# Kernel optimization log

Measured on AMD Instinct MI355X. Metric: run time of the kernel, lower is better.

The kernel has to match this reference:

```python
import jax, jax.numpy as jnp
import numpy as np

TAU = 250.0   # tau_inv used by all behaviours (norse default / explicit for LLBN)
DT = 0.001
VTH = 30.0
T_STEPS = 10000

# (a, b, c, d) Izhikevich params per cell
LLBN_P = (0.1, -0.075, -55.0, 6.0)      # custom spiking behaviour
EBN_P = (0.02, 0.25, -55.0, 0.05)       # phasic_bursting
IFN_P = (0.02, 0.25, -65.0, 6.0)        # phasic_spiking
TN_P = (0.02, 0.2, -65.0, 6.0)          # tonic_spiking
MN_P = (0.02, 0.25, -65.0, 6.0)         # phasic_spiking


def setup_inputs() -> dict:
    key = jax.random.key(0)
    k1, k2 = jax.random.split(key)
    input_mat = jax.random.uniform(k1, (127, 127), dtype=jnp.float32)
    weights_matrix = jax.random.uniform(k2, (12,), dtype=jnp.float32)
    return {"input_mat": input_mat, "weights_matrix": weights_matrix,
            "nb_repetitions": T_STEPS}


def _izh(v, u, I, p):
    a, b, c, d = p
    v1 = v + TAU * DT * (0.04 * v * v + 5.0 * v + 140.0 - u + I)
    u1 = u + TAU * DT * a * (b * v - u)
    z = (v1 >= VTH).astype(v.dtype)
    return z, jnp.where(z > 0, c, v1), u1 + z * d


def _simulate(input_mat, w, nb_repetitions):
    z_plus = jnp.sum(input_mat * w[0])  # constant across timesteps

    def step(carry, _):
        temp, z2p, v2, u2, v3, u3, v4, u4, z5p, v5, u5, v6, u6 = carry
        # LLBN: recurrent cell, input current = w2*(z_plus*w1 - temp) + w3*z_prev
        z2, v2, u2 = _izh(v2, u2, w[2] * (z_plus * w[1] - temp) + w[3] * z2p, LLBN_P)
        # EBN
        z3, v3, u3 = _izh(v3, u3, z_plus * w[4] + z2 * w[5], EBN_P)
        # IFN (feedback to LLBN via temp, one-step delay)
        z4, v4, u4 = _izh(v4, u4, z3 * w[6], IFN_P)
        temp_n = z4 * w[7]
        # TN: recurrent cell, input current = w9*(z3*w8) + w10*z_prev
        z5, v5, u5 = _izh(v5, u5, w[9] * (z3 * w[8]) + w[10] * z5p, TN_P)
        # MN
        z6, v6, u6 = _izh(v6, u6, z5 * w[11], MN_P)
        new_carry = (temp_n, z2, v2, u2, v3, u3, v4, u4, z5, v5, u5, v6, u6)
        out = (jnp.stack([z2, z3, z4, z5, z6]),  # spikes [5]
               jnp.stack([v2, v3, v4, v5, v6]))  # membrane voltages [5]
        return new_carry, out

    f32 = jnp.float32
    init = (f32(0.0),                      # temp
            f32(0.0), f32(-60.0), f32(4.5),    # LLBN z, v, u (u0 = b*v_rest)
            f32(-64.0), f32(-16.0),            # EBN v, u
            f32(-64.0), f32(-16.0),            # IFN v, u
            f32(0.0), f32(-70.0), f32(-14.0),  # TN z, v, u
            f32(-64.0), f32(-16.0))            # MN v, u
    _, (spikes, volts) = jax.lax.scan(step, init, None, length=nb_repetitions)
    return spikes.T, volts.T  # each [5, T]


def reference(input_mat, weights_matrix, nb_repetitions):
    o_spikes, v = _simulate(input_mat, weights_matrix, nb_repetitions)
    return o_spikes, v
```

## Files before the change

kernel.cpp:

```cpp
#include <hip/hip_runtime.h>

#pragma clang fp contract(off)


__global__ __launch_bounds__(256) void net_sim(const float* __restrict__ mat,
                                               const float* __restrict__ w,
                                               float* __restrict__ out,
                                               int* __restrict__ ws,
                                               int T) {
    __shared__ double red[256];
    const int tid = threadIdx.x;

    const float w0 = w[0];
    double s = 0.0;
    for (int i = tid; i < 127 * 127; i += 256) {
        float p = mat[i] * w0;
        s += (double)p;
    }
    red[tid] = s;
    __syncthreads();
    #pragma unroll
    for (int off = 128; off > 0; off >>= 1) {
        if (tid < off) red[tid] += red[tid + off];
        __syncthreads();
    }
    if (tid >= 9) return;

    const float z_plus = (float)red[0];

    const float w2 = w[2], w3 = w[3], w5 = w[5], w6 = w[6], w7 = w[7],
                w8 = w[8], w9 = w[9], w10 = w[10], w11 = w[11];
    const float zp_w1 = z_plus * w[1];
    const float zp_w4 = z_plus * w[4];

    const float I2_00 = w2 * (zp_w1 - 0.0f) + w3 * 0.0f;
    const float I2_10 = w2 * (zp_w1 - 0.0f) + w3 * 1.0f;
    const float I2_01 = w2 * (zp_w1 - w7)   + w3 * 0.0f;
    const float I2_11 = w2 * (zp_w1 - w7)   + w3 * 1.0f;
    const float I3_0  = zp_w4 + 0.0f * w5;
    const float I3_1  = zp_w4 + 1.0f * w5;
    const float I4_0  = 0.0f * w6;
    const float I4_1  = 1.0f * w6;
    const float I5_00 = w9 * (0.0f * w8) + w10 * 0.0f;
    const float I5_10 = w9 * (1.0f * w8) + w10 * 0.0f;
    const float I5_01 = w9 * (0.0f * w8) + w10 * 1.0f;
    const float I5_11 = w9 * (1.0f * w8) + w10 * 1.0f;
    const float I6_0  = 0.0f * w11;
    const float I6_1  = 1.0f * w11;

    const int lane = tid;
    const int g = lane == 0 ? 0 : lane <= 2 ? 1 : lane <= 4 ? 2 : lane <= 6 ? 3 : 4;

    const float ka = lane == 0 ? (float)(0.25 * 0.1) : (float)(0.25 * 0.02);
    const float b  = lane == 0 ? -0.075f : (g == 3 ? 0.2f : 0.25f);
    const float c  = g <= 1 ? -55.0f : -65.0f;
    const float d  = g == 1 ? 0.05f : 6.0f;
    float v = g == 0 ? -60.0f : (g == 3 ? -70.0f : -64.0f);
    float u = g == 0 ? 4.5f   : (g == 3 ? -14.0f : -16.0f);

    const float C0a = g == 0 ? I2_00 : g == 1 ? I3_0 : g == 2 ? I4_0
                    : g == 3 ? I5_00 : I6_0;
    const float C0b = g == 0 ? I2_00 : g == 1 ? I3_0 : g == 2 ? I4_0
                    : g == 3 ? I5_01 : I6_0;
    const float C1a = g == 1 ? I3_1 : g == 2 ? I4_1 : g == 3 ? I5_10
                    : g == 4 ? I6_1 : 0.0f;
    const float C1b = g == 1 ? I3_1 : g == 2 ? I4_1 : g == 3 ? I5_11
                    : g == 4 ? I6_1 : 0.0f;

    const bool is_lane0  = (lane == 0);
    const bool spec_var1 = (lane == 2) | (lane == 4) | (lane == 6) | (lane == 8);
    const unsigned lanebit = 1u << lane;

    float* __restrict__ psp = out + g * T;
    float* __restrict__ pvv = out + 5 * T + g * T;

    int z2 = 0, z4 = 0, z5 = 0;

    float av = 0.0f, au = 0.0f;
    int az2 = 0, az4 = 0, az5 = 0;
    int anchor_t = -1, next_anchor = 8;
    int t_det = -1, Pf = 0;

    float zb[8], vb[8];

    int t = 0;
    for (; t + 8 <= T; t += 8) {
        if (t == next_anchor) {
            av = v; au = u; az2 = z2; az4 = z4; az5 = z5;
            anchor_t = t; next_anchor <<= 1;
        } else if (anchor_t >= 0) {
            unsigned long long mv =
                __ballot(__float_as_uint(v) == __float_as_uint(av));
            unsigned long long mu =
                __ballot(__float_as_uint(u) == __float_as_uint(au));
            if (((mv & mu) & 0x1FFull) == 0x1FFull &&
                z2 == az2 && z4 == az4 && z5 == az5) {
                t_det = t; Pf = t - anchor_t;
                break;
            }
        }

        #pragma unroll
        for (int j = 0; j < 8; ++j) {
            float fI2 = z4 ? (z2 ? I2_11 : I2_01) : (z2 ? I2_10 : I2_00);
            float V0 = z5 ? C0b : C0a;
            float V1 = z5 ? C1b : C1a;
            V0 = is_lane0 ? fI2 : V0;
            float Ib = spec_var1 ? V1 : V0;

            float t1 = 0.04f * v;
            float t2 = t1 * v;
            float t3 = 5.0f * v;
            float t4 = t2 + t3;
            float t5 = t4 + 140.0f;
            float t6 = t5 - u;
            float bv = b * v;
            float bvu = bv - u;
            float du = ka * bvu;
            float u1 = u + du;

            float t7b = t6 + Ib;
            float dvb = 0.25f * t7b;
            float v1b = v + dvb;
            unsigned long long m = __ballot(v1b >= 30.0f);

            int nz2 = (int)(m & 1ull);
            int z3  = (int)((m >> (1 + nz2)) & 1ull);
            int nz4 = (int)((m >> (3 + z3)) & 1ull);
            int nz5 = (int)((m >> (5 + z3)) & 1ull);
            unsigned ssel = (nz2 ? 0x006u : 0u) | (z3 ? 0x078u : 0u)
                          | (nz5 ? 0x180u : 0u);

            bool asel = (ssel & lanebit) != 0u;
            float Ia = asel ? V1 : V0;
            float t7a = t6 + Ia;
            float dva = 0.25f * t7a;
            float v1a = v + dva;
            bool fa = (v1a >= 30.0f);
            v = fa ? c : v1a;
            float u1d = u1 + d;
            u = fa ? u1d : u1;

            zb[j] = fa ? 1.0f : 0.0f;
            vb[j] = v;

            z2 = nz2; z4 = nz4; z5 = nz5;
        }
        *(float4*)(psp)     = make_float4(zb[0], zb[1], zb[2], zb[3]);
        *(float4*)(psp + 4) = make_float4(zb[4], zb[5], zb[6], zb[7]);
        *(float4*)(pvv)     = make_float4(vb[0], vb[1], vb[2], vb[3]);
        *(float4*)(pvv + 4) = make_float4(vb[4], vb[5], vb[6], vb[7]);
        psp += 8;
        pvv += 8;
    }
    for (; t < T && t_det < 0; ++t) {
        float fI2 = z4 ? (z2 ? I2_11 : I2_01) : (z2 ? I2_10 : I2_00);
        float V0 = z5 ? C0b : C0a;
        float V1 = z5 ? C1b : C1a;
        V0 = is_lane0 ? fI2 : V0;
        float Ib = spec_var1 ? V1 : V0;
        float t1 = 0.04f * v;
        float t2 = t1 * v;
        float t3 = 5.0f * v;
        float t4 = t2 + t3;
        float t5 = t4 + 140.0f;
        float t6 = t5 - u;
        float bv = b * v;
        float bvu = bv - u;
        float du = ka * bvu;
        float u1 = u + du;
        float t7b = t6 + Ib;
        float dvb = 0.25f * t7b;
        float v1b = v + dvb;
        unsigned long long m = __ballot(v1b >= 30.0f);
        int nz2 = (int)(m & 1ull);
        int z3  = (int)((m >> (1 + nz2)) & 1ull);
        int nz4 = (int)((m >> (3 + z3)) & 1ull);
        int nz5 = (int)((m >> (5 + z3)) & 1ull);
        unsigned ssel = (nz2 ? 0x006u : 0u) | (z3 ? 0x078u : 0u)
                      | (nz5 ? 0x180u : 0u);
        bool asel = (ssel & lanebit) != 0u;
        float Ia = asel ? V1 : V0;
        float t7a = t6 + Ia;
        float dva = 0.25f * t7a;
        float v1a = v + dva;
        bool fa = (v1a >= 30.0f);
        v = fa ? c : v1a;
        float u1d = u1 + d;
        u = fa ? u1d : u1;
        psp[0] = fa ? 1.0f : 0.0f;
        pvv[0] = v;
        ++psp; ++pvv;
        z2 = nz2; z4 = nz4; z5 = nz5;
    }

    if (lane == 0) {
        ws[0] = (t_det >= 0) ? 1 : 0;
        ws[1] = t_det;
        ws[2] = Pf;
    }
}

__global__ __launch_bounds__(256) void fill_cycle(float* __restrict__ out,
                                                  const int* __restrict__ ws,
                                                  int T) {
    if (ws[0] == 0) return;
    const int t0 = ws[1];
    const int P  = ws[2];
    const int r  = blockIdx.y;
    const float* __restrict__ src = out + (size_t)r * T + (t0 - P);
    float* __restrict__ dst       = out + (size_t)r * T + t0;
    const int n = T - t0;
    for (int i = blockIdx.x * blockDim.x + threadIdx.x; i < n;
         i += gridDim.x * blockDim.x) {
        dst[i] = src[i % P];
    }
}

extern "C" void kernel_launch(void* const* d_in, const int* in_sizes, int n_in,
                              void* d_out, int out_size, void* d_ws, size_t ws_size,
                              hipStream_t stream) {
    const float* mat = (const float*)d_in[0];
    const float* w   = (const float*)d_in[1];
    int T = out_size / 10;
    net_sim<<<1, 256, 0, stream>>>(mat, w, (float*)d_out, (int*)d_ws, T);
    dim3 grid(40, 10, 1);
    fill_cycle<<<grid, 256, 0, stream>>>((float*)d_out, (const int*)d_ws, T);
}
```

Baseline: 346.1 us.

## Use one lane per cell with dual-input speculation and add periodic fine cycle anchors

Each of the 5 neurons now runs on a single lane. Every lane evaluates both possible input currents, and two ballots resolve the spike chain as scalar SGPR masks; v_cndmask inline asm then applies the selections with no per-lane recomputation. This replaces the 9-lane speculative layout and its second dependent v1 computation plus compare. Cycle detection gains a fine anchor every 64 steps alongside the doubling coarse anchor, so a periodic steady state can be found earlier and the remaining outputs filled by copying. The cost is an extra pair of ballots and compares in each 8-step check.

```diff
diff --git a/kernel.cpp b/kernel.cpp
--- a/kernel.cpp
+++ b/kernel.cpp
@@ -2,6 +2,12 @@
 
 #pragma clang fp contract(off)
 
+
+__device__ __forceinline__ float sel_mask(float a, float b, unsigned long long m) {
+    float r;
+    asm("v_cndmask_b32 %0, %1, %2, %3" : "=v"(r) : "v"(a), "v"(b), "s"(m));
+    return r;
+}
 
 __global__ __launch_bounds__(256) void net_sim(const float* __restrict__ mat,
                                                const float* __restrict__ w,
@@ -24,7 +30,7 @@
         if (tid < off) red[tid] += red[tid + off];
         __syncthreads();
     }
-    if (tid >= 9) return;
+    if (tid >= 5) return;
 
     const float z_plus = (float)red[0];
 
@@ -49,64 +55,68 @@
     const float I6_1  = 1.0f * w11;
 
     const int lane = tid;
-    const int g = lane == 0 ? 0 : lane <= 2 ? 1 : lane <= 4 ? 2 : lane <= 6 ? 3 : 4;
-
     const float ka = lane == 0 ? (float)(0.25 * 0.1) : (float)(0.25 * 0.02);
-    const float b  = lane == 0 ? -0.075f : (g == 3 ? 0.2f : 0.25f);
-    const float c  = g <= 1 ? -55.0f : -65.0f;
-    const float d  = g == 1 ? 0.05f : 6.0f;
-    float v = g == 0 ? -60.0f : (g == 3 ? -70.0f : -64.0f);
-    float u = g == 0 ? 4.5f   : (g == 3 ? -14.0f : -16.0f);
-
-    const float C0a = g == 0 ? I2_00 : g == 1 ? I3_0 : g == 2 ? I4_0
-                    : g == 3 ? I5_00 : I6_0;
-    const float C0b = g == 0 ? I2_00 : g == 1 ? I3_0 : g == 2 ? I4_0
-                    : g == 3 ? I5_01 : I6_0;
-    const float C1a = g == 1 ? I3_1 : g == 2 ? I4_1 : g == 3 ? I5_10
-                    : g == 4 ? I6_1 : 0.0f;
-    const float C1b = g == 1 ? I3_1 : g == 2 ? I4_1 : g == 3 ? I5_11
-                    : g == 4 ? I6_1 : 0.0f;
-
-    const bool is_lane0  = (lane == 0);
-    const bool spec_var1 = (lane == 2) | (lane == 4) | (lane == 6) | (lane == 8);
-    const unsigned lanebit = 1u << lane;
-
-    float* __restrict__ psp = out + g * T;
-    float* __restrict__ pvv = out + 5 * T + g * T;
+    const float b  = lane == 0 ? -0.075f : (lane == 3 ? 0.2f : 0.25f);
+    const float cc = lane <= 1 ? -55.0f : -65.0f;
+    const float d  = lane == 1 ? 0.05f : 6.0f;
+    float v = lane == 0 ? -60.0f : (lane == 3 ? -70.0f : -64.0f);
+    float u = lane == 0 ? 4.5f   : (lane == 3 ? -14.0f : -16.0f);
+
+    const float K0a = lane == 1 ? I3_0 : lane == 2 ? I4_0 : lane == 3 ? I5_00
+                    : lane == 4 ? I6_0 : 0.0f;
+    const float K0b = lane == 3 ? I5_01 : K0a;
+    const float K1a = lane == 1 ? I3_1 : lane == 2 ? I4_1 : lane == 3 ? I5_10
+                    : lane == 4 ? I6_1 : 0.0f;
+    const float K1b = lane == 3 ? I5_11 : K1a;
+    const bool is_l0 = (lane == 0);
+
+    float* __restrict__ psp = out + lane * T;
+    float* __restrict__ pvv = out + 5 * T + lane * T;
 
     int z2 = 0, z4 = 0, z5 = 0;
 
-    float av = 0.0f, au = 0.0f;
-    int az2 = 0, az4 = 0, az5 = 0;
-    int anchor_t = -1, next_anchor = 8;
+    float fav = 0.0f, fau = 0.0f; int faz2 = 0, faz4 = 0, faz5 = 0, fa_t = -1;
+    float cav = 0.0f, cau = 0.0f; int caz2 = 0, caz4 = 0, caz5 = 0, ca_t = -1;
+    int next_coarse = 8;
     int t_det = -1, Pf = 0;
 
     float zb[8], vb[8];
 
     int t = 0;
     for (; t + 8 <= T; t += 8) {
-        if (t == next_anchor) {
-            av = v; au = u; az2 = z2; az4 = z4; az5 = z5;
-            anchor_t = t; next_anchor <<= 1;
-        } else if (anchor_t >= 0) {
+        int hitA = -1;
+        if (fa_t >= 0) {
             unsigned long long mv =
-                __ballot(__float_as_uint(v) == __float_as_uint(av));
+                __ballot(__float_as_uint(v) == __float_as_uint(fav));
             unsigned long long mu =
-                __ballot(__float_as_uint(u) == __float_as_uint(au));
-            if (((mv & mu) & 0x1FFull) == 0x1FFull &&
-                z2 == az2 && z4 == az4 && z5 == az5) {
-                t_det = t; Pf = t - anchor_t;
-                break;
-            }
+                __ballot(__float_as_uint(u) == __float_as_uint(fau));
+            if (((mv & mu) & 0x1Full) == 0x1Full &&
+                z2 == faz2 && z4 == faz4 && z5 == faz5) hitA = fa_t;
+        }
+        if (hitA < 0 && ca_t >= 0) {
+            unsigned long long mv =
+                __ballot(__float_as_uint(v) == __float_as_uint(cav));
+            unsigned long long mu =
+                __ballot(__float_as_uint(u) == __float_as_uint(cau));
+            if (((mv & mu) & 0x1Full) == 0x1Full &&
+                z2 == caz2 && z4 == caz4 && z5 == caz5) hitA = ca_t;
+        }
+        if (hitA >= 0) { t_det = t; Pf = t - hitA; break; }
+        if ((t & 63) == 0 && t) {
+            fav = v; fau = u; faz2 = z2; faz4 = z4; faz5 = z5; fa_t = t;
+        }
+        if (t == next_coarse) {
+            cav = v; cau = u; caz2 = z2; caz4 = z4; caz5 = z5; ca_t = t;
+            next_coarse <<= 1;
         }
 
         #pragma unroll
         for (int j = 0; j < 8; ++j) {
             float fI2 = z4 ? (z2 ? I2_11 : I2_01) : (z2 ? I2_10 : I2_00);
-            float V0 = z5 ? C0b : C0a;
-            float V1 = z5 ? C1b : C1a;
-            V0 = is_lane0 ? fI2 : V0;
-            float Ib = spec_var1 ? V1 : V0;
+            float J0 = z5 ? K0b : K0a;
+            float J1 = z5 ? K1b : K1a;
+            J0 = is_l0 ? fI2 : J0;
+            J1 = is_l0 ? fI2 : J1;
 
             float t1 = 0.04f * v;
             float t2 = t1 * v;
@@ -118,30 +128,36 @@
             float bvu = bv - u;
             float du = ka * bvu;
             float u1 = u + du;
-
-            float t7b = t6 + Ib;
-            float dvb = 0.25f * t7b;
-            float v1b = v + dvb;
-            unsigned long long m = __ballot(v1b >= 30.0f);
-
-            int nz2 = (int)(m & 1ull);
-            int z3  = (int)((m >> (1 + nz2)) & 1ull);
-            int nz4 = (int)((m >> (3 + z3)) & 1ull);
-            int nz5 = (int)((m >> (5 + z3)) & 1ull);
-            unsigned ssel = (nz2 ? 0x006u : 0u) | (z3 ? 0x078u : 0u)
-                          | (nz5 ? 0x180u : 0u);
-
-            bool asel = (ssel & lanebit) != 0u;
-            float Ia = asel ? V1 : V0;
-            float t7a = t6 + Ia;
-            float dva = 0.25f * t7a;
-            float v1a = v + dva;
-            bool fa = (v1a >= 30.0f);
-            v = fa ? c : v1a;
             float u1d = u1 + d;
-            u = fa ? u1d : u1;
-
-            zb[j] = fa ? 1.0f : 0.0f;
+
+            float t7_0 = t6 + J0;
+            float dv_0 = 0.25f * t7_0;
+            float v1_0 = v + dv_0;
+            float t7_1 = t6 + J1;
+            float dv_1 = 0.25f * t7_1;
+            float v1_1 = v + dv_1;
+            unsigned long long m0 = __ballot(v1_0 >= 30.0f);
+            unsigned long long m1 = __ballot(v1_1 >= 30.0f);
+
+            int nz2 = (int)(m0 & 1ull);
+            unsigned long long me = nz2 ? m1 : m0;
+            int z3  = (int)((me >> 1) & 1ull);
+            unsigned long long mi = z3 ? m1 : m0;
+            int nz4 = (int)((mi >> 2) & 1ull);
+            int nz5 = (int)((mi >> 3) & 1ull);
+            unsigned long long mm = nz5 ? m1 : m0;
+            int nz6 = (int)((mm >> 4) & 1ull);
+
+            unsigned long long act = (nz2 ? 0x02ull : 0ull) |
+                                     (z3  ? 0x0Cull : 0ull) |
+                                     (nz5 ? 0x10ull : 0ull);
+            unsigned long long fam = (unsigned long long)(nz2 | (z3 << 1) |
+                                     (nz4 << 2) | (nz5 << 3) | (nz6 << 4));
+
+            float v1a = sel_mask(v1_0, v1_1, act);
+            v = sel_mask(v1a, cc, fam);
+            u = sel_mask(u1, u1d, fam);
+            zb[j] = sel_mask(0.0f, 1.0f, fam);
             vb[j] = v;
 
             z2 = nz2; z4 = nz4; z5 = nz5;
@@ -155,10 +171,10 @@
     }
     for (; t < T && t_det < 0; ++t) {
         float fI2 = z4 ? (z2 ? I2_11 : I2_01) : (z2 ? I2_10 : I2_00);
-        float V0 = z5 ? C0b : C0a;
-        float V1 = z5 ? C1b : C1a;
-        V0 = is_lane0 ? fI2 : V0;
-        float Ib = spec_var1 ? V1 : V0;
+        float J0 = z5 ? K0b : K0a;
+        float J1 = z5 ? K1b : K1a;
+        J0 = is_l0 ? fI2 : J0;
+        J1 = is_l0 ? fI2 : J1;
         float t1 = 0.04f * v;
         float t2 = t1 * v;
         float t3 = 5.0f * v;
@@ -169,26 +185,32 @@
         float bvu = bv - u;
         float du = ka * bvu;
         float u1 = u + du;
-        float t7b = t6 + Ib;
-        float dvb = 0.25f * t7b;
-        float v1b = v + dvb;
-        unsigned long long m = __ballot(v1b >= 30.0f);
-        int nz2 = (int)(m & 1ull);
-        int z3  = (int)((m >> (1 + nz2)) & 1ull);
-        int nz4 = (int)((m >> (3 + z3)) & 1ull);
-        int nz5 = (int)((m >> (5 + z3)) & 1ull);
-        unsigned ssel = (nz2 ? 0x006u : 0u) | (z3 ? 0x078u : 0u)
-                      | (nz5 ? 0x180u : 0u);
-        bool asel = (ssel & lanebit) != 0u;
-        float Ia = asel ? V1 : V0;
-        float t7a = t6 + Ia;
-        float dva = 0.25f * t7a;
-        float v1a = v + dva;
-        bool fa = (v1a >= 30.0f);
-        v = fa ? c : v1a;
         float u1d = u1 + d;
-        u = fa ? u1d : u1;
-        psp[0] = fa ? 1.0f : 0.0f;
+        float t7_0 = t6 + J0;
+        float dv_0 = 0.25f * t7_0;
+        float v1_0 = v + dv_0;
+        float t7_1 = t6 + J1;
+        float dv_1 = 0.25f * t7_1;
+        float v1_1 = v + dv_1;
+        unsigned long long m0 = __ballot(v1_0 >= 30.0f);
+        unsigned long long m1 = __ballot(v1_1 >= 30.0f);
+        int nz2 = (int)(m0 & 1ull);
+        unsigned long long me = nz2 ? m1 : m0;
+        int z3  = (int)((me >> 1) & 1ull);
+        unsigned long long mi = z3 ? m1 : m0;
+        int nz4 = (int)((mi >> 2) & 1ull);
+        int nz5 = (int)((mi >> 3) & 1ull);
+        unsigned long long mm = nz5 ? m1 : m0;
+        int nz6 = (int)((mm >> 4) & 1ull);
+        unsigned long long act = (nz2 ? 0x02ull : 0ull) |
+                                 (z3  ? 0x0Cull : 0ull) |
+                                 (nz5 ? 0x10ull : 0ull);
+        unsigned long long fam = (unsigned long long)(nz2 | (z3 << 1) |
+                                 (nz4 << 2) | (nz5 << 3) | (nz6 << 4));
+        float v1a = sel_mask(v1_0, v1_1, act);
+        v = sel_mask(v1a, cc, fam);
+        u = sel_mask(u1, u1d, fam);
+        psp[0] = sel_mask(0.0f, 1.0f, fam);
         pvv[0] = v;
         ++psp; ++pvv;
         z2 = nz2; z4 = nz4; z5 = nz5;
```

After: 328.4 us. -5.1%, faster.

## Add periodic-40 anchor for cycle detection and use SGPR-mask lane select

Applied to the files above, without the earlier changes.

Adds a second cycle-detection anchor that re-anchors every 40 steps and checks at those points, alongside the existing power-of-two anchor. This catches steady-state periods that divide 40 much earlier than the doubling anchor does, so the serial simulation can stop sooner and hand the rest to the fill kernel. It also replaces the per-lane bit test with an inline-asm v_cndmask driven by a scalar 64-bit mask, which shortens the serial critical path of each step. Risks include inline asm constraints forcing extra moves, and detection that is only valid when the state repeats exactly.

```diff
diff --git a/kernel.cpp b/kernel.cpp
--- a/kernel.cpp
+++ b/kernel.cpp
@@ -2,6 +2,12 @@
 
 #pragma clang fp contract(off)
 
+
+__device__ __forceinline__ float sel_mask(float a, float b, unsigned long long m) {
+    float r;
+    asm("v_cndmask_b32 %0, %1, %2, %3" : "=v"(r) : "v"(a), "v"(b), "s"(m));
+    return r;
+}
 
 __global__ __launch_bounds__(256) void net_sim(const float* __restrict__ mat,
                                                const float* __restrict__ w,
@@ -69,35 +75,48 @@
 
     const bool is_lane0  = (lane == 0);
     const bool spec_var1 = (lane == 2) | (lane == 4) | (lane == 6) | (lane == 8);
-    const unsigned lanebit = 1u << lane;
 
     float* __restrict__ psp = out + g * T;
     float* __restrict__ pvv = out + 5 * T + g * T;
 
     int z2 = 0, z4 = 0, z5 = 0;
 
-    float av = 0.0f, au = 0.0f;
-    int az2 = 0, az4 = 0, az5 = 0;
-    int anchor_t = -1, next_anchor = 8;
+    float rav = 0.0f, rau = 0.0f; int raz2 = 0, raz4 = 0, raz5 = 0, ra_t = -1;
+    float cav = 0.0f, cau = 0.0f; int caz2 = 0, caz4 = 0, caz5 = 0, ca_t = -1;
+    int next_coarse = 8;
     int t_det = -1, Pf = 0;
 
     float zb[8], vb[8];
 
     int t = 0;
     for (; t + 8 <= T; t += 8) {
-        if (t == next_anchor) {
-            av = v; au = u; az2 = z2; az4 = z4; az5 = z5;
-            anchor_t = t; next_anchor <<= 1;
-        } else if (anchor_t >= 0) {
+        if (t % 40 == 0) {
+            if (ra_t >= 0) {
+                unsigned long long mv =
+                    __ballot(__float_as_uint(v) == __float_as_uint(rav));
+                unsigned long long mu =
+                    __ballot(__float_as_uint(u) == __float_as_uint(rau));
+                if (((mv & mu) & 0x1FFull) == 0x1FFull &&
+                    z2 == raz2 && z4 == raz4 && z5 == raz5) {
+                    t_det = t; Pf = t - ra_t;
+                    break;
+                }
+            }
+            if (t) { rav = v; rau = u; raz2 = z2; raz4 = z4; raz5 = z5; ra_t = t; }
+        } else if (ca_t >= 0) {
             unsigned long long mv =
-                __ballot(__float_as_uint(v) == __float_as_uint(av));
+                __ballot(__float_as_uint(v) == __float_as_uint(cav));
             unsigned long long mu =
-                __ballot(__float_as_uint(u) == __float_as_uint(au));
+                __ballot(__float_as_uint(u) == __float_as_uint(cau));
             if (((mv & mu) & 0x1FFull) == 0x1FFull &&
-                z2 == az2 && z4 == az4 && z5 == az5) {
-                t_det = t; Pf = t - anchor_t;
+                z2 == caz2 && z4 == caz4 && z5 == caz5) {
+                t_det = t; Pf = t - ca_t;
                 break;
             }
+        }
+        if (t == next_coarse) {
+            cav = v; cau = u; caz2 = z2; caz4 = z4; caz5 = z5; ca_t = t;
+            next_coarse <<= 1;
         }
 
         #pragma unroll
@@ -128,11 +147,11 @@
             int z3  = (int)((m >> (1 + nz2)) & 1ull);
             int nz4 = (int)((m >> (3 + z3)) & 1ull);
             int nz5 = (int)((m >> (5 + z3)) & 1ull);
-            unsigned ssel = (nz2 ? 0x006u : 0u) | (z3 ? 0x078u : 0u)
-                          | (nz5 ? 0x180u : 0u);
-
-            bool asel = (ssel & lanebit) != 0u;
-            float Ia = asel ? V1 : V0;
+            unsigned long long ssel =
+                (nz2 ? 0x006ull : 0ull) | (z3 ? 0x078ull : 0ull)
+              | (nz5 ? 0x180ull : 0ull);
+
+            float Ia = sel_mask(V0, V1, ssel);
             float t7a = t6 + Ia;
             float dva = 0.25f * t7a;
             float v1a = v + dva;
@@ -177,10 +196,10 @@
         int z3  = (int)((m >> (1 + nz2)) & 1ull);
         int nz4 = (int)((m >> (3 + z3)) & 1ull);
         int nz5 = (int)((m >> (5 + z3)) & 1ull);
-        unsigned ssel = (nz2 ? 0x006u : 0u) | (z3 ? 0x078u : 0u)
-                      | (nz5 ? 0x180u : 0u);
-        bool asel = (ssel & lanebit) != 0u;
-        float Ia = asel ? V1 : V0;
+        unsigned long long ssel =
+            (nz2 ? 0x006ull : 0ull) | (z3 ? 0x078ull : 0ull)
+          | (nz5 ? 0x180ull : 0ull);
+        float Ia = sel_mask(V0, V1, ssel);
         float t7a = t6 + Ia;
         float dva = 0.25f * t7a;
         float v1a = v + dva;
```

Result: faster. 305.2 us (-11.8%).
